# Performance work log

Hardware: AMD Instinct MI355X
Metric: run time of the kernel (lower is better)

Reference implementation:

```python
import jax, jax.numpy as jnp
import numpy as np

NEG_MAX = -jnp.finfo(jnp.float32).max


def apply_rotary(x):
    # x: (b, h, n, d) with d = key_dim; interleaved rotary (lucidrains rotary-embedding-torch)
    d = x.shape[-1]
    n = x.shape[-2]
    inv_freq = 1.0 / (10000.0 ** (jnp.arange(0, d, 2, dtype=jnp.float32) / d))
    t = jnp.arange(n, dtype=jnp.float32)
    freqs = t[:, None] * inv_freq[None, :]              # (n, d/2)
    cos, sin = jnp.cos(freqs), jnp.sin(freqs)
    x1, x2 = x[..., 0::2], x[..., 1::2]                 # even/odd interleaved pairs
    out1 = x1 * cos - x2 * sin
    out2 = x1 * sin + x2 * cos
    return jnp.stack([out1, out2], axis=-1).reshape(x.shape)


def setup_inputs() -> dict:
    key = jax.random.key(0)
    ks = jax.random.split(key, 12)
    b, n, dim, de = 2, 1024, 256, 64
    h, kd, vd = 8, 32, 32
    node_in = jax.random.normal(ks[0], (b, n, dim), dtype=jnp.float32)
    edge_in = jax.random.normal(ks[1], (b, n, n, de), dtype=jnp.float32)
    mask = jax.random.randint(ks[2], (b, n), 0, 2).astype(bool)
    s = 1.0 / np.sqrt(dim)
    Wq = jax.random.normal(ks[3], (dim, h * kd), dtype=jnp.float32) * s
    Wk = jax.random.normal(ks[4], (dim, h * kd), dtype=jnp.float32) * s
    Wv = jax.random.normal(ks[5], (dim, h * vd), dtype=jnp.float32) * s
    We = jax.random.normal(ks[6], (de, h), dtype=jnp.float32) * (1.0 / np.sqrt(de))
    be = jax.random.normal(ks[7], (h,), dtype=jnp.float32) * 0.01
    Wo = jax.random.normal(ks[8], (h * (vd + de), dim), dtype=jnp.float32) * (1.0 / np.sqrt(h * (vd + de)))
    bo = jax.random.normal(ks[9], (dim,), dtype=jnp.float32) * 0.01
    return {"node_in": node_in, "edge_in": edge_in, "mask": mask,
            "Wq": Wq, "Wk": Wk, "Wv": Wv, "We": We, "be": be, "Wo": Wo, "bo": bo}


def reference(node_in, edge_in, mask, Wq, Wk, Wv, We, be, Wo, bo):
    b, n, dim = node_in.shape
    h = be.shape[0]
    kd = Wq.shape[1] // h
    vd = Wv.shape[1] // h
    num_attn_logits = 2
    node_scale = (num_attn_logits * kd) ** -0.5
    edge_scale = num_attn_logits ** -0.5

    # projections -> (b, h, n, d)
    def proj(W, d):
        return (node_in @ W).reshape(b, n, h, d).transpose(0, 2, 1, 3)
    q, k, v = proj(Wq, kd), proj(Wk, kd), proj(Wv, vd)
    q, k = apply_rotary(q), apply_rotary(k)

    logits = jnp.einsum('bhid,bhjd->bhij', q, k) * node_scale
    edge_bias = (jnp.einsum('bijd,dh->bijh', edge_in, We) + be)  # (b, n, n, h)
    logits = logits + edge_bias.transpose(0, 3, 1, 2) * edge_scale

    pair_mask = mask[:, :, None] & mask[:, None, :]              # (b, n, n)
    logits = jnp.where(pair_mask[:, None, :, :], logits, NEG_MAX)

    attn = jax.nn.softmax(logits, axis=-1)                       # (b, h, n, n)

    res_node = jnp.einsum('bhij,bhjd->bhid', attn, v)            # (b, h, n, vd)
    res_edge = jnp.einsum('bhij,bijd->bhid', attn, edge_in)      # (b, h, n, de)

    res_node = res_node.transpose(0, 2, 1, 3).reshape(b, n, h * vd)
    res_edge = res_edge.transpose(0, 2, 1, 3).reshape(b, n, -1)
    out = jnp.concatenate([res_node, res_edge], axis=-1) @ Wo + bo
    return out
```

## Files before the change

kernel.cpp:

```cpp
#include <hip/hip_runtime.h>
#include <hip/hip_bf16.h>

typedef float f32x4 __attribute__((ext_vector_type(4)));
typedef short short8 __attribute__((ext_vector_type(8)));
typedef unsigned short u16;
typedef unsigned int u32;
typedef unsigned int u32x4 __attribute__((ext_vector_type(4)));

#define NEG_MAX (-3.4028234663852886e38f)
#define NODE_SCALE 0.125f
#define EDGE_SCALE 0.70710678118654752f
#define TSTR 68

__device__ __forceinline__ u16 f2bf(float f) {
  unsigned int x = __builtin_bit_cast(unsigned int, f);
  x = x + 0x7FFFu + ((x >> 16) & 1u);
  return (u16)(x >> 16);
}
__device__ __forceinline__ float asf(u32 x) { return __builtin_bit_cast(float, x); }
__device__ __forceinline__ u32 cvtpk(float lo, float hi) {
  u32 r;
  asm("v_cvt_pk_bf16_f32 %0, %1, %2" : "=v"(r) : "v"(lo), "v"(hi));
  return r;
}

__global__ void mask_norm(const unsigned char* __restrict__ mraw,
                          float* __restrict__ mask_f) {
  __shared__ int flags;
  int t = threadIdx.x;
  if (t == 0) flags = 0;
  __syncthreads();
  const unsigned int* mu = (const unsigned int*)mraw;
  int f = 0;
  for (int e = t; e < 512; e += 256) { if (mu[e] > 1u) f |= 1; }
  for (int e = t; e < 2048; e += 256) { if (mraw[e] > 1) f |= 2; }
  if (f) atomicOr(&flags, f);
  __syncthreads();
  int fl = flags;
  for (int e = t; e < 2048; e += 256) {
    float v;
    if (!(fl & 1))      v = (mu[e] != 0u) ? 1.f : 0.f;
    else if (!(fl & 2)) v = (mraw[e] != 0) ? 1.f : 0.f;
    else                v = (((const float*)mraw)[e] != 0.f) ? 1.f : 0.f;
    mask_f[e] = v;
  }
}

__global__ __launch_bounds__(256) void qkv_rope(
    const float* __restrict__ node, const float* __restrict__ Wq,
    const float* __restrict__ Wk, const float* __restrict__ Wv,
    float* __restrict__ qw, u16* __restrict__ kwb, u16* __restrict__ vwb) {
  __shared__ __align__(16) float xs[8 * 256];
  int t = threadIdx.x;
  int row0 = blockIdx.x * 8;
#pragma unroll
  for (int p = 0; p < 2; ++p) {
    int f = p * 256 + t;
    *(f32x4*)(&xs[f * 4]) = *(const f32x4*)(node + (size_t)row0 * 256 + f * 4);
  }
  __syncthreads();
  float qa[8], ka[8], va[8];
#pragma unroll
  for (int r = 0; r < 8; ++r) { qa[r] = 0.f; ka[r] = 0.f; va[r] = 0.f; }
  for (int c = 0; c < 256; ++c) {
    float wq = Wq[c * 256 + t];
    float wk = Wk[c * 256 + t];
    float wv = Wv[c * 256 + t];
#pragma unroll
    for (int r = 0; r < 8; ++r) {
      float x = xs[r * 256 + c];
      qa[r] += x * wq; ka[r] += x * wk; va[r] += x * wv;
    }
  }
  int d = t & 31;
  float inv = powf(10000.f, -((float)(2 * (d >> 1)) * (1.f / 32.f)));
  int h = t >> 5;
#pragma unroll
  for (int r = 0; r < 8; ++r) {
    int gr = row0 + r;
    int b = gr >> 10, i = gr & 1023;
    float ang = (float)i * inv;
    float sn, cs;
    sincosf(ang, &sn, &cs);
    float qp = __shfl_xor(qa[r], 1, 64);
    float kp = __shfl_xor(ka[r], 1, 64);
    float qo = (d & 1) ? (qp * sn + qa[r] * cs) : (qa[r] * cs - qp * sn);
    float ko = (d & 1) ? (kp * sn + ka[r] * cs) : (ka[r] * cs - kp * sn);
    int idx = ((b * 8 + h) * 1024 + i) * 32 + d;
    qw[idx] = qo;
    kwb[idx] = f2bf(ko);
    vwb[idx] = f2bf(va[r]);
  }
}

#define WREG 1280
__global__ __launch_bounds__(256) void attn_fused(
    const float* __restrict__ edge, const float* __restrict__ qw,
    const u16* __restrict__ kwb, const u16* __restrict__ vwb,
    const float* __restrict__ We, const float* __restrict__ be,
    const float* __restrict__ mask_f, float* __restrict__ rescat) {
  __shared__ __align__(16) float S[4 * WREG];

  int bid = blockIdx.x;
  int xcd = bid & 7, slot = bid >> 3;
  int b = xcd >> 2;
  int i = (xcd & 3) * 256 + slot;
  int t = threadIdx.x;
  int lane = t & 63;
  int w = __builtin_amdgcn_readfirstlane(t >> 6);

  float* tile = S + w * WREG;
  float* Pf = tile + 1088;
  float* Rg = tile + 1248;

  int j16 = lane & 15;
  int hq = lane >> 4;
  int hD = lane >> 3, sD = lane & 7;
  int jrl = lane >> 2, c4 = lane & 3;
  int jh = sD >> 2, do4 = sD & 3;

  float mi = mask_f[b * 1024 + i];
  u32 mb = 0;
  if (mi != 0.f) {
#pragma unroll
    for (int tt = 0; tt < 16; ++tt) {
      float v = mask_f[b * 1024 + tt * 64 + w * 16 + j16];
      mb |= (v != 0.f ? 1u : 0u) << tt;
    }
  }
  f32x4 besq = *(const f32x4*)(be + (hq & 1) * 4);
  besq *= EDGE_SCALE;

  short8 weA0, weA1;
  {
    int hh = lane & 15, g = lane >> 4;
#pragma unroll
    for (int e = 0; e < 8; ++e) {
      int d0 = g * 8 + e;
      float w0 = (hh < 8) ? We[d0 * 8 + hh] * EDGE_SCALE : 0.f;
      float w1 = (hh < 8) ? We[(d0 + 32) * 8 + hh] * EDGE_SCALE : 0.f;
      weA0[e] = (short)f2bf(w0);
      weA1[e] = (short)f2bf(w1);
    }
  }

  short8 qA[8];
  {
    int hh = (lane & 15) & 7;
    const float* qp = qw + ((size_t)((b * 8 + hh) * 1024 + i)) * 32 + (lane >> 4) * 8;
    f32x4 qv0 = *(const f32x4*)(qp);
    f32x4 qv1 = *(const f32x4*)(qp + 4);
    qv0 *= NODE_SCALE;
    qv1 *= NODE_SCALE;
    u32x4 qpk;
    qpk[0] = cvtpk(qv0.x, qv0.y); qpk[1] = cvtpk(qv0.z, qv0.w);
    qpk[2] = cvtpk(qv1.x, qv1.y); qpk[3] = cvtpk(qv1.z, qv1.w);
    u32x4 zz = {0u, 0u, 0u, 0u};
#pragma unroll
    for (int h = 0; h < 8; ++h)
      qA[h] = __builtin_bit_cast(short8, ((lane & 15) == h) ? qpk : zz);
  }

  const float* ebase = edge + ((size_t)(b * 1024 + i)) * (1024 * 64);
  const float* gsrc = ebase + (size_t)(w * 16 + jrl) * 64 + c4 * 16;
  float* wdst = tile + jrl * TSTR + c4 * 16;

  {
    f32x4 a0 = __builtin_nontemporal_load((const f32x4*)(gsrc + 0));
    f32x4 a1 = __builtin_nontemporal_load((const f32x4*)(gsrc + 4));
    f32x4 a2 = __builtin_nontemporal_load((const f32x4*)(gsrc + 8));
    f32x4 a3 = __builtin_nontemporal_load((const f32x4*)(gsrc + 12));
    *(f32x4*)(wdst + 0) = a0;
    *(f32x4*)(wdst + 4) = a1;
    *(f32x4*)(wdst + 8) = a2;
    *(f32x4*)(wdst + 12) = a3;
  }

  f32x4 vm = {NEG_MAX, NEG_MAX, NEG_MAX, NEG_MAX};
  f32x4 vs = {0.f, 0.f, 0.f, 0.f};
  f32x4 av0 = {0.f, 0.f, 0.f, 0.f}, av1 = {0.f, 0.f, 0.f, 0.f};
  f32x4 acce0 = {0.f, 0.f, 0.f, 0.f}, acce1 = {0.f, 0.f, 0.f, 0.f};
  f32x4 acce2 = {0.f, 0.f, 0.f, 0.f}, acce3 = {0.f, 0.f, 0.f, 0.f};

  for (int tt = 0; tt < 16; ++tt) {
    int j0 = tt * 64;
    bool pf = tt < 15;
    f32x4 st0, st1, st2, st3;
    if (pf) {
      const float* g = gsrc + (size_t)(j0 + 64) * 64;
      st0 = __builtin_nontemporal_load((const f32x4*)(g + 0));
      st1 = __builtin_nontemporal_load((const f32x4*)(g + 4));
      st2 = __builtin_nontemporal_load((const f32x4*)(g + 8));
      st3 = __builtin_nontemporal_load((const f32x4*)(g + 12));
    }

    f32x4 bacc = {0.f, 0.f, 0.f, 0.f};
    {
      const float* rp = tile + j16 * TSTR + hq * 8;
      f32x4 ea0 = *(const f32x4*)(rp + 0);
      f32x4 ea1 = *(const f32x4*)(rp + 4);
      f32x4 eb0 = *(const f32x4*)(rp + 32);
      f32x4 eb1 = *(const f32x4*)(rp + 36);
      u32x4 p0, p1;
      p0[0] = cvtpk(ea0.x, ea0.y); p0[1] = cvtpk(ea0.z, ea0.w);
      p0[2] = cvtpk(ea1.x, ea1.y); p0[3] = cvtpk(ea1.z, ea1.w);
      p1[0] = cvtpk(eb0.x, eb0.y); p1[1] = cvtpk(eb0.z, eb0.w);
      p1[2] = cvtpk(eb1.x, eb1.y); p1[3] = cvtpk(eb1.z, eb1.w);
      bacc = __builtin_amdgcn_mfma_f32_16x16x32_bf16(
          weA0, __builtin_bit_cast(short8, p0), bacc, 0, 0, 0);
      bacc = __builtin_amdgcn_mfma_f32_16x16x32_bf16(
          weA1, __builtin_bit_cast(short8, p1), bacc, 0, 0, 0);
    }
#pragma unroll
    for (int h = 0; h < 8; ++h) {
      const u16* kp = kwb + ((size_t)((b * 8 + h) * 1024 + j0 + w * 16 + j16)) * 32 + hq * 8;
      short8 kB = *(const short8*)kp;
      bacc = __builtin_amdgcn_mfma_f32_16x16x32_bf16(qA[h], kB, bacc, 0, 0, 0);
    }

    f32x4 p;
    {
      bool pm = (mb >> tt) & 1u;
      f32x4 l;
#pragma unroll
      for (int r = 0; r < 4; ++r) l[r] = pm ? (bacc[r] + besq[r]) : NEG_MAX;
      f32x4 mx = l;
#pragma unroll
      for (int off = 1; off < 16; off <<= 1) {
#pragma unroll
        for (int r = 0; r < 4; ++r) mx[r] = fmaxf(mx[r], __shfl_xor(mx[r], off, 64));
      }
      f32x4 mn, rs;
#pragma unroll
      for (int r = 0; r < 4; ++r) {
        mn[r] = fmaxf(vm[r], mx[r]);
        p[r] = __expf(l[r] - mn[r]);
      }
      f32x4 ps = p;
#pragma unroll
      for (int off = 1; off < 16; off <<= 1) {
#pragma unroll
        for (int r = 0; r < 4; ++r) ps[r] += __shfl_xor(ps[r], off, 64);
      }
#pragma unroll
      for (int r = 0; r < 4; ++r) rs[r] = __expf(vm[r] - mn[r]);
      vs = vs * rs + ps;
      vm = mn;
      if (lane < 32) {
        float* pw = Pf + hq * 80 + j16;
        pw[0] = p[0]; pw[20] = p[1]; pw[40] = p[2]; pw[60] = p[3];
        if (j16 == 0) *(f32x4*)(Rg + hq * 4) = rs;
      }
    }

    {
      float r = Rg[hD];
      const float* prow = Pf + hD * 20;
      f32x4 pr0 = *(const f32x4*)(prow + 0);
      f32x4 pr1 = *(const f32x4*)(prow + 4);
      f32x4 pr2 = *(const f32x4*)(prow + 8);
      f32x4 pr3 = *(const f32x4*)(prow + 12);
      const u16* vb = vwb + ((size_t)((b * 8 + hD) * 1024 + j0 + w * 16 + jh * 8)) * 32 + do4 * 8;
      f32x4 prA = jh ? pr2 : pr0, prB = jh ? pr3 : pr1;
      f32x4 sv0 = {0.f, 0.f, 0.f, 0.f}, sv1 = {0.f, 0.f, 0.f, 0.f};
#pragma unroll
      for (int x = 0; x < 8; ++x) {
        float pv = (x < 4) ? prA[x] : prB[x - 4];
        u32x4 vv = *(const u32x4*)(vb + (size_t)x * 32);
        f32x4 e0 = {asf(vv[0] << 16), asf(vv[0] & 0xffff0000u),
                    asf(vv[1] << 16), asf(vv[1] & 0xffff0000u)};
        f32x4 e1 = {asf(vv[2] << 16), asf(vv[2] & 0xffff0000u),
                    asf(vv[3] << 16), asf(vv[3] & 0xffff0000u)};
        sv0 += e0 * pv;
        sv1 += e1 * pv;
      }
      av0 = av0 * r + sv0;
      av1 = av1 * r + sv1;
    }

    {
      f32x4 rgv = *(const f32x4*)(Rg + (hq & 1) * 4);
      const float* pArow = Pf + (lane & 7) * 20 + (hq & 1) * 8;
      f32x4 pa0 = *(const f32x4*)(pArow);
      f32x4 pa1 = *(const f32x4*)(pArow + 4);
      u32x4 apk;
      apk[0] = cvtpk(pa0.x, pa0.y); apk[1] = cvtpk(pa0.z, pa0.w);
      apk[2] = cvtpk(pa1.x, pa1.y); apk[3] = cvtpk(pa1.z, pa1.w);
      if (hq >= 2) apk = (u32x4){0u, 0u, 0u, 0u};
      short8 pAf = __builtin_bit_cast(short8, apk);
      const float* cb = tile + (hq & 1) * 8 * TSTR + j16;
#define PE_STEP(ACC, NT) {                                                   \
      float b0 = cb[(NT)*16 + 0*TSTR], b1 = cb[(NT)*16 + 1*TSTR];            \
      float b2 = cb[(NT)*16 + 2*TSTR], b3 = cb[(NT)*16 + 3*TSTR];            \
      float b4 = cb[(NT)*16 + 4*TSTR], b5 = cb[(NT)*16 + 5*TSTR];            \
      float b6 = cb[(NT)*16 + 6*TSTR], b7 = cb[(NT)*16 + 7*TSTR];            \
      u32x4 bpk;                                                             \
      bpk[0] = cvtpk(b0, b1); bpk[1] = cvtpk(b2, b3);                        \
      bpk[2] = cvtpk(b4, b5); bpk[3] = cvtpk(b6, b7);                        \
      ACC = ACC * rgv;                                                       \
      ACC = __builtin_amdgcn_mfma_f32_16x16x32_bf16(                         \
          pAf, __builtin_bit_cast(short8, bpk), ACC, 0, 0, 0); }
      PE_STEP(acce0, 0)
      PE_STEP(acce1, 1)
      PE_STEP(acce2, 2)
      PE_STEP(acce3, 3)
#undef PE_STEP
    }

    if (pf) {
      *(f32x4*)(wdst + 0) = st0;
      *(f32x4*)(wdst + 4) = st1;
      *(f32x4*)(wdst + 8) = st2;
      *(f32x4*)(wdst + 12) = st3;
    }
  }

  __syncthreads();
  float* mrg = S + w * 1040;
  if (lane < 32) {
    int h0 = hq * 4;
    if (j16 == 0) {
#pragma unroll
      for (int r = 0; r < 4; ++r) { mrg[h0 + r] = vm[r]; mrg[8 + h0 + r] = vs[r]; }
    }
#pragma unroll
    for (int r = 0; r < 4; ++r) {
      mrg[528 + (h0 + r) * 64 + 0 + j16] = acce0[r];
      mrg[528 + (h0 + r) * 64 + 16 + j16] = acce1[r];
      mrg[528 + (h0 + r) * 64 + 32 + j16] = acce2[r];
      mrg[528 + (h0 + r) * 64 + 48 + j16] = acce3[r];
    }
  }
  *(f32x4*)(mrg + 16 + jh * 256 + hD * 32 + do4 * 8) = av0;
  *(f32x4*)(mrg + 16 + jh * 256 + hD * 32 + do4 * 8 + 4) = av1;
  __syncthreads();
  {
    int h = t >> 5, d = t & 31;
    float mx = fmaxf(fmaxf(S[h], S[1040 + h]), fmaxf(S[2080 + h], S[3120 + h]));
    float ew[4];
    float ssum = 0.f, vsum = 0.f;
#pragma unroll
    for (int ww = 0; ww < 4; ++ww) {
      const float* mw = S + ww * 1040;
      ew[ww] = __expf(mw[h] - mx);
      ssum += mw[8 + h] * ew[ww];
      vsum += (mw[16 + h * 32 + d] + mw[16 + 256 + h * 32 + d]) * ew[ww];
    }
    float inv = 1.f / ssum;
    size_t obase = ((size_t)(b * 1024 + i)) * 768;
    rescat[obase + h * 32 + d] = vsum * inv;
    float e0 = 0.f, e1 = 0.f;
#pragma unroll
    for (int ww = 0; ww < 4; ++ww) {
      const float* mw = S + ww * 1040;
      e0 += mw[528 + h * 64 + d] * ew[ww];
      e1 += mw[528 + h * 64 + 32 + d] * ew[ww];
    }
    rescat[obase + 256 + h * 64 + d] = e0 * inv;
    rescat[obase + 256 + h * 64 + 32 + d] = e1 * inv;
  }
}

__global__ __launch_bounds__(256) void out_proj(
    const float* __restrict__ rescat, const float* __restrict__ Wo,
    const float* __restrict__ bo, float* __restrict__ out) {
  __shared__ __align__(16) float xs[8 * 768];
  int t = threadIdx.x;
  int row0 = blockIdx.x * 8;
#pragma unroll
  for (int p = 0; p < 6; ++p) {
    int f = p * 256 + t;
    *(f32x4*)(&xs[f * 4]) = *(const f32x4*)(rescat + (size_t)row0 * 768 + f * 4);
  }
  __syncthreads();
  float acc[8];
#pragma unroll
  for (int r = 0; r < 8; ++r) acc[r] = 0.f;
  for (int c = 0; c < 768; ++c) {
    float w = Wo[c * 256 + t];
#pragma unroll
    for (int r = 0; r < 8; ++r) acc[r] += xs[r * 768 + c] * w;
  }
  float bias = bo[t];
#pragma unroll
  for (int r = 0; r < 8; ++r)
    out[(size_t)(row0 + r) * 256 + t] = acc[r] + bias;
}

extern "C" void kernel_launch(void* const* d_in, const int* in_sizes, int n_in,
                              void* d_out, int out_size, void* d_ws, size_t ws_size,
                              hipStream_t stream) {
  const float* node = (const float*)d_in[0];
  const float* edge = (const float*)d_in[1];
  const unsigned char* mask = (const unsigned char*)d_in[2];
  const float* Wq = (const float*)d_in[3];
  const float* Wk = (const float*)d_in[4];
  const float* Wv = (const float*)d_in[5];
  const float* We = (const float*)d_in[6];
  const float* be = (const float*)d_in[7];
  const float* Wo = (const float*)d_in[8];
  const float* bo = (const float*)d_in[9];

  float* ws = (float*)d_ws;
  float* qw = ws;
  u16* kwb = (u16*)(ws + 524288);
  u16* vwb = kwb + 524288;
  float* rescat = ws + 1048576;
  float* mask_f = ws + 2621440;

  hipLaunchKernelGGL(mask_norm, dim3(1), dim3(256), 0, stream, mask, mask_f);
  hipLaunchKernelGGL(qkv_rope, dim3(256), dim3(256), 0, stream,
                     node, Wq, Wk, Wv, qw, kwb, vwb);
  hipLaunchKernelGGL(attn_fused, dim3(2048), dim3(256), 0, stream,
                     edge, qw, kwb, vwb, We, be, mask_f, rescat);
  hipLaunchKernelGGL(out_proj, dim3(256), dim3(256), 0, stream,
                     rescat, Wo, bo, (float*)d_out);
}
```

Before: 393.8 us.

## Process two key tiles per online-softmax step with doubled edge prefetch

After: 402.3 us. 1.02x slower.

```diff
diff --git a/kernel.cpp b/kernel.cpp
--- a/kernel.cpp
+++ b/kernel.cpp
@@ -11,6 +11,8 @@
 #define NODE_SCALE 0.125f
 #define EDGE_SCALE 0.70710678118654752f
 #define TSTR 68
+#define PSTR 36
+#define WREG 2496
 
 __device__ __forceinline__ u16 f2bf(float f) {
   unsigned int x = __builtin_bit_cast(unsigned int, f);
@@ -93,7 +95,6 @@
   }
 }
 
-#define WREG 1280
 __global__ __launch_bounds__(256) void attn_fused(
     const float* __restrict__ edge, const float* __restrict__ qw,
     const u16* __restrict__ kwb, const u16* __restrict__ vwb,
@@ -109,9 +110,11 @@
   int lane = t & 63;
   int w = __builtin_amdgcn_readfirstlane(t >> 6);
 
-  float* tile = S + w * WREG;
-  float* Pf = tile + 1088;
-  float* Rg = tile + 1248;
+  float* base = S + w * WREG;
+  float* tA = base;
+  float* tB = base + 1088;
+  float* Pf = base + 2176;
+  float* Rg = base + 2464;
 
   int j16 = lane & 15;
   int hq = lane >> 4;
@@ -163,17 +166,23 @@
 
   const float* ebase = edge + ((size_t)(b * 1024 + i)) * (1024 * 64);
   const float* gsrc = ebase + (size_t)(w * 16 + jrl) * 64 + c4 * 16;
-  float* wdst = tile + jrl * TSTR + c4 * 16;
 
   {
     f32x4 a0 = __builtin_nontemporal_load((const f32x4*)(gsrc + 0));
     f32x4 a1 = __builtin_nontemporal_load((const f32x4*)(gsrc + 4));
     f32x4 a2 = __builtin_nontemporal_load((const f32x4*)(gsrc + 8));
     f32x4 a3 = __builtin_nontemporal_load((const f32x4*)(gsrc + 12));
-    *(f32x4*)(wdst + 0) = a0;
-    *(f32x4*)(wdst + 4) = a1;
-    *(f32x4*)(wdst + 8) = a2;
-    *(f32x4*)(wdst + 12) = a3;
+    const float* g2 = gsrc + 64 * 64;
+    f32x4 b0 = __builtin_nontemporal_load((const f32x4*)(g2 + 0));
+    f32x4 b1 = __builtin_nontemporal_load((const f32x4*)(g2 + 4));
+    f32x4 b2 = __builtin_nontemporal_load((const f32x4*)(g2 + 8));
+    f32x4 b3 = __builtin_nontemporal_load((const f32x4*)(g2 + 12));
+    float* wa = tA + jrl * TSTR + c4 * 16;
+    float* wb = tB + jrl * TSTR + c4 * 16;
+    *(f32x4*)(wa + 0) = a0; *(f32x4*)(wa + 4) = a1;
+    *(f32x4*)(wa + 8) = a2; *(f32x4*)(wa + 12) = a3;
+    *(f32x4*)(wb + 0) = b0; *(f32x4*)(wb + 4) = b1;
+    *(f32x4*)(wb + 8) = b2; *(f32x4*)(wb + 12) = b3;
   }
 
   f32x4 vm = {NEG_MAX, NEG_MAX, NEG_MAX, NEG_MAX};
@@ -182,21 +191,31 @@
   f32x4 acce0 = {0.f, 0.f, 0.f, 0.f}, acce1 = {0.f, 0.f, 0.f, 0.f};
   f32x4 acce2 = {0.f, 0.f, 0.f, 0.f}, acce3 = {0.f, 0.f, 0.f, 0.f};
 
-  for (int tt = 0; tt < 16; ++tt) {
-    int j0 = tt * 64;
-    bool pf = tt < 15;
-    f32x4 st0, st1, st2, st3;
+  for (int m = 0; m < 8; ++m) {
+    int j0 = m * 128;
+    bool pf = m < 7;
+    f32x4 sA0, sA1, sA2, sA3, sB0, sB1, sB2, sB3;
     if (pf) {
-      const float* g = gsrc + (size_t)(j0 + 64) * 64;
-      st0 = __builtin_nontemporal_load((const f32x4*)(g + 0));
-      st1 = __builtin_nontemporal_load((const f32x4*)(g + 4));
-      st2 = __builtin_nontemporal_load((const f32x4*)(g + 8));
-      st3 = __builtin_nontemporal_load((const f32x4*)(g + 12));
-    }
-
-    f32x4 bacc = {0.f, 0.f, 0.f, 0.f};
+      const float* gA = gsrc + (size_t)(j0 + 128) * 64;
+      const float* gB = gsrc + (size_t)(j0 + 192) * 64;
+      sA0 = __builtin_nontemporal_load((const f32x4*)(gA + 0));
+      sA1 = __builtin_nontemporal_load((const f32x4*)(gA + 4));
+      sA2 = __builtin_nontemporal_load((const f32x4*)(gA + 8));
+      sA3 = __builtin_nontemporal_load((const f32x4*)(gA + 12));
+      sB0 = __builtin_nontemporal_load((const f32x4*)(gB + 0));
+      sB1 = __builtin_nontemporal_load((const f32x4*)(gB + 4));
+      sB2 = __builtin_nontemporal_load((const f32x4*)(gB + 8));
+      sB3 = __builtin_nontemporal_load((const f32x4*)(gB + 12));
+    }
+
+    short8 kA[8];
+#pragma unroll
+    for (int h = 0; h < 8; ++h)
+      kA[h] = *(const short8*)(kwb +
+          ((size_t)((b * 8 + h) * 1024 + j0 + w * 16 + j16)) * 32 + hq * 8);
+    f32x4 baccA = {0.f, 0.f, 0.f, 0.f};
     {
-      const float* rp = tile + j16 * TSTR + hq * 8;
+      const float* rp = tA + j16 * TSTR + hq * 8;
       f32x4 ea0 = *(const f32x4*)(rp + 0);
       f32x4 ea1 = *(const f32x4*)(rp + 4);
       f32x4 eb0 = *(const f32x4*)(rp + 32);
@@ -206,37 +225,64 @@
       p0[2] = cvtpk(ea1.x, ea1.y); p0[3] = cvtpk(ea1.z, ea1.w);
       p1[0] = cvtpk(eb0.x, eb0.y); p1[1] = cvtpk(eb0.z, eb0.w);
       p1[2] = cvtpk(eb1.x, eb1.y); p1[3] = cvtpk(eb1.z, eb1.w);
-      bacc = __builtin_amdgcn_mfma_f32_16x16x32_bf16(
-          weA0, __builtin_bit_cast(short8, p0), bacc, 0, 0, 0);
-      bacc = __builtin_amdgcn_mfma_f32_16x16x32_bf16(
-          weA1, __builtin_bit_cast(short8, p1), bacc, 0, 0, 0);
-    }
-#pragma unroll
-    for (int h = 0; h < 8; ++h) {
-      const u16* kp = kwb + ((size_t)((b * 8 + h) * 1024 + j0 + w * 16 + j16)) * 32 + hq * 8;
-      short8 kB = *(const short8*)kp;
-      bacc = __builtin_amdgcn_mfma_f32_16x16x32_bf16(qA[h], kB, bacc, 0, 0, 0);
-    }
-
-    f32x4 p;
+      baccA = __builtin_amdgcn_mfma_f32_16x16x32_bf16(
+          weA0, __builtin_bit_cast(short8, p0), baccA, 0, 0, 0);
+      baccA = __builtin_amdgcn_mfma_f32_16x16x32_bf16(
+          weA1, __builtin_bit_cast(short8, p1), baccA, 0, 0, 0);
+    }
+#pragma unroll
+    for (int h = 0; h < 8; ++h)
+      baccA = __builtin_amdgcn_mfma_f32_16x16x32_bf16(qA[h], kA[h], baccA, 0, 0, 0);
+
+    short8 kB[8];
+#pragma unroll
+    for (int h = 0; h < 8; ++h)
+      kB[h] = *(const short8*)(kwb +
+          ((size_t)((b * 8 + h) * 1024 + j0 + 64 + w * 16 + j16)) * 32 + hq * 8);
+    f32x4 baccB = {0.f, 0.f, 0.f, 0.f};
     {
-      bool pm = (mb >> tt) & 1u;
-      f32x4 l;
-#pragma unroll
-      for (int r = 0; r < 4; ++r) l[r] = pm ? (bacc[r] + besq[r]) : NEG_MAX;
-      f32x4 mx = l;
+      const float* rp = tB + j16 * TSTR + hq * 8;
+      f32x4 ea0 = *(const f32x4*)(rp + 0);
+      f32x4 ea1 = *(const f32x4*)(rp + 4);
+      f32x4 eb0 = *(const f32x4*)(rp + 32);
+      f32x4 eb1 = *(const f32x4*)(rp + 36);
+      u32x4 p0, p1;
+      p0[0] = cvtpk(ea0.x, ea0.y); p0[1] = cvtpk(ea0.z, ea0.w);
+      p0[2] = cvtpk(ea1.x, ea1.y); p0[3] = cvtpk(ea1.z, ea1.w);
+      p1[0] = cvtpk(eb0.x, eb0.y); p1[1] = cvtpk(eb0.z, eb0.w);
+      p1[2] = cvtpk(eb1.x, eb1.y); p1[3] = cvtpk(eb1.z, eb1.w);
+      baccB = __builtin_amdgcn_mfma_f32_16x16x32_bf16(
+          weA0, __builtin_bit_cast(short8, p0), baccB, 0, 0, 0);
+      baccB = __builtin_amdgcn_mfma_f32_16x16x32_bf16(
+          weA1, __builtin_bit_cast(short8, p1), baccB, 0, 0, 0);
+    }
+#pragma unroll
+    for (int h = 0; h < 8; ++h)
+      baccB = __builtin_amdgcn_mfma_f32_16x16x32_bf16(qA[h], kB[h], baccB, 0, 0, 0);
+
+    {
+      bool pmA = (mb >> (2 * m)) & 1u;
+      bool pmB = (mb >> (2 * m + 1)) & 1u;
+      f32x4 lA, lB, pA, pB, mx;
+#pragma unroll
+      for (int r = 0; r < 4; ++r) {
+        lA[r] = pmA ? (baccA[r] + besq[r]) : NEG_MAX;
+        lB[r] = pmB ? (baccB[r] + besq[r]) : NEG_MAX;
+        mx[r] = fmaxf(lA[r], lB[r]);
+      }
 #pragma unroll
       for (int off = 1; off < 16; off <<= 1) {
 #pragma unroll
         for (int r = 0; r < 4; ++r) mx[r] = fmaxf(mx[r], __shfl_xor(mx[r], off, 64));
       }
-      f32x4 mn, rs;
+      f32x4 mn, rs, ps;
 #pragma unroll
       for (int r = 0; r < 4; ++r) {
         mn[r] = fmaxf(vm[r], mx[r]);
-        p[r] = __expf(l[r] - mn[r]);
-      }
-      f32x4 ps = p;
+        pA[r] = __expf(lA[r] - mn[r]);
+        pB[r] = __expf(lB[r] - mn[r]);
+        ps[r] = pA[r] + pB[r];
+      }
 #pragma unroll
       for (int off = 1; off < 16; off <<= 1) {
 #pragma unroll
@@ -247,26 +293,35 @@
       vs = vs * rs + ps;
       vm = mn;
       if (lane < 32) {
-        float* pw = Pf + hq * 80 + j16;
-        pw[0] = p[0]; pw[20] = p[1]; pw[40] = p[2]; pw[60] = p[3];
+        float* pw = Pf + hq * (4 * PSTR) + j16;
+        pw[0 * PSTR] = pA[0]; pw[1 * PSTR] = pA[1];
+        pw[2 * PSTR] = pA[2]; pw[3 * PSTR] = pA[3];
+        pw[0 * PSTR + 16] = pB[0]; pw[1 * PSTR + 16] = pB[1];
+        pw[2 * PSTR + 16] = pB[2]; pw[3 * PSTR + 16] = pB[3];
         if (j16 == 0) *(f32x4*)(Rg + hq * 4) = rs;
       }
     }
 
     {
       float r = Rg[hD];
-      const float* prow = Pf + hD * 20;
-      f32x4 pr0 = *(const f32x4*)(prow + 0);
-      f32x4 pr1 = *(const f32x4*)(prow + 4);
-      f32x4 pr2 = *(const f32x4*)(prow + 8);
-      f32x4 pr3 = *(const f32x4*)(prow + 12);
-      const u16* vb = vwb + ((size_t)((b * 8 + hD) * 1024 + j0 + w * 16 + jh * 8)) * 32 + do4 * 8;
-      f32x4 prA = jh ? pr2 : pr0, prB = jh ? pr3 : pr1;
+      const float* prow = Pf + hD * PSTR;
+      f32x4 a0 = *(const f32x4*)(prow + 0);
+      f32x4 a1 = *(const f32x4*)(prow + 4);
+      f32x4 a2 = *(const f32x4*)(prow + 8);
+      f32x4 a3 = *(const f32x4*)(prow + 12);
+      f32x4 b0 = *(const f32x4*)(prow + 16);
+      f32x4 b1 = *(const f32x4*)(prow + 20);
+      f32x4 b2 = *(const f32x4*)(prow + 24);
+      f32x4 b3 = *(const f32x4*)(prow + 28);
+      f32x4 prA = jh ? a2 : a0, prA2 = jh ? a3 : a1;
+      f32x4 prB = jh ? b2 : b0, prB2 = jh ? b3 : b1;
+      const u16* vbA = vwb + ((size_t)((b * 8 + hD) * 1024 + j0 + w * 16 + jh * 8)) * 32 + do4 * 8;
+      const u16* vbB = vbA + (size_t)64 * 32;
       f32x4 sv0 = {0.f, 0.f, 0.f, 0.f}, sv1 = {0.f, 0.f, 0.f, 0.f};
 #pragma unroll
       for (int x = 0; x < 8; ++x) {
-        float pv = (x < 4) ? prA[x] : prB[x - 4];
-        u32x4 vv = *(const u32x4*)(vb + (size_t)x * 32);
+        float pv = (x < 4) ? prA[x] : prA2[x - 4];
+        u32x4 vv = *(const u32x4*)(vbA + (size_t)x * 32);
         f32x4 e0 = {asf(vv[0] << 16), asf(vv[0] & 0xffff0000u),
                     asf(vv[1] << 16), asf(vv[1] & 0xffff0000u)};
         f32x4 e1 = {asf(vv[2] << 16), asf(vv[2] & 0xffff0000u),
@@ -274,44 +329,72 @@
         sv0 += e0 * pv;
         sv1 += e1 * pv;
       }
+#pragma unroll
+      for (int x = 0; x < 8; ++x) {
+        float pv = (x < 4) ? prB[x] : prB2[x - 4];
+        u32x4 vv = *(const u32x4*)(vbB + (size_t)x * 32);
+        f32x4 e0 = {asf(vv[0] << 16), asf(vv[0] & 0xffff0000u),
+                    asf(vv[1] << 16), asf(vv[1] & 0xffff0000u)};
+        f32x4 e1 = {asf(vv[2] << 16), asf(vv[2] & 0xffff0000u),
+                    asf(vv[3] << 16), asf(vv[3] & 0xffff0000u)};
+        sv0 += e0 * pv;
+        sv1 += e1 * pv;
+      }
       av0 = av0 * r + sv0;
       av1 = av1 * r + sv1;
     }
 
     {
       f32x4 rgv = *(const f32x4*)(Rg + (hq & 1) * 4);
-      const float* pArow = Pf + (lane & 7) * 20 + (hq & 1) * 8;
-      f32x4 pa0 = *(const f32x4*)(pArow);
-      f32x4 pa1 = *(const f32x4*)(pArow + 4);
-      u32x4 apk;
-      apk[0] = cvtpk(pa0.x, pa0.y); apk[1] = cvtpk(pa0.z, pa0.w);
-      apk[2] = cvtpk(pa1.x, pa1.y); apk[3] = cvtpk(pa1.z, pa1.w);
-      if (hq >= 2) apk = (u32x4){0u, 0u, 0u, 0u};
-      short8 pAf = __builtin_bit_cast(short8, apk);
-      const float* cb = tile + (hq & 1) * 8 * TSTR + j16;
-#define PE_STEP(ACC, NT) {                                                   \
-      float b0 = cb[(NT)*16 + 0*TSTR], b1 = cb[(NT)*16 + 1*TSTR];            \
-      float b2 = cb[(NT)*16 + 2*TSTR], b3 = cb[(NT)*16 + 3*TSTR];            \
-      float b4 = cb[(NT)*16 + 4*TSTR], b5 = cb[(NT)*16 + 5*TSTR];            \
-      float b6 = cb[(NT)*16 + 6*TSTR], b7 = cb[(NT)*16 + 7*TSTR];            \
-      u32x4 bpk;                                                             \
-      bpk[0] = cvtpk(b0, b1); bpk[1] = cvtpk(b2, b3);                        \
-      bpk[2] = cvtpk(b4, b5); bpk[3] = cvtpk(b6, b7);                        \
+      const float* pAr = Pf + (lane & 7) * PSTR + (hq & 1) * 8;
+      f32x4 pa0 = *(const f32x4*)(pAr);
+      f32x4 pa1 = *(const f32x4*)(pAr + 4);
+      f32x4 pb0 = *(const f32x4*)(pAr + 16);
+      f32x4 pb1 = *(const f32x4*)(pAr + 20);
+      u32x4 apkA, apkB;
+      apkA[0] = cvtpk(pa0.x, pa0.y); apkA[1] = cvtpk(pa0.z, pa0.w);
+      apkA[2] = cvtpk(pa1.x, pa1.y); apkA[3] = cvtpk(pa1.z, pa1.w);
+      apkB[0] = cvtpk(pb0.x, pb0.y); apkB[1] = cvtpk(pb0.z, pb0.w);
+      apkB[2] = cvtpk(pb1.x, pb1.y); apkB[3] = cvtpk(pb1.z, pb1.w);
+      if (hq >= 2) { apkA = (u32x4){0u,0u,0u,0u}; apkB = (u32x4){0u,0u,0u,0u}; }
+      short8 pAfA = __builtin_bit_cast(short8, apkA);
+      short8 pAfB = __builtin_bit_cast(short8, apkB);
+      const float* cbA = tA + (hq & 1) * 8 * TSTR + j16;
+      const float* cbB = tB + (hq & 1) * 8 * TSTR + j16;
+#define PE_STEP2(ACC, NT) {                                                  \
+      float a0_ = cbA[(NT)*16 + 0*TSTR], a1_ = cbA[(NT)*16 + 1*TSTR];        \
+      float a2_ = cbA[(NT)*16 + 2*TSTR], a3_ = cbA[(NT)*16 + 3*TSTR];        \
+      float a4_ = cbA[(NT)*16 + 4*TSTR], a5_ = cbA[(NT)*16 + 5*TSTR];        \
+      float a6_ = cbA[(NT)*16 + 6*TSTR], a7_ = cbA[(NT)*16 + 7*TSTR];        \
+      u32x4 bka;                                                             \
+      bka[0] = cvtpk(a0_, a1_); bka[1] = cvtpk(a2_, a3_);                    \
+      bka[2] = cvtpk(a4_, a5_); bka[3] = cvtpk(a6_, a7_);                    \
+      float b0_ = cbB[(NT)*16 + 0*TSTR], b1_ = cbB[(NT)*16 + 1*TSTR];        \
+      float b2_ = cbB[(NT)*16 + 2*TSTR], b3_ = cbB[(NT)*16 + 3*TSTR];        \
+      float b4_ = cbB[(NT)*16 + 4*TSTR], b5_ = cbB[(NT)*16 + 5*TSTR];        \
+      float b6_ = cbB[(NT)*16 + 6*TSTR], b7_ = cbB[(NT)*16 + 7*TSTR];        \
+      u32x4 bkb;                                                             \
+      bkb[0] = cvtpk(b0_, b1_); bkb[1] = cvtpk(b2_, b3_);                    \
+      bkb[2] = cvtpk(b4_, b5_); bkb[3] = cvtpk(b6_, b7_);                    \
       ACC = ACC * rgv;                                                       \
       ACC = __builtin_amdgcn_mfma_f32_16x16x32_bf16(                         \
-          pAf, __builtin_bit_cast(short8, bpk), ACC, 0, 0, 0); }
-      PE_STEP(acce0, 0)
-      PE_STEP(acce1, 1)
-      PE_STEP(acce2, 2)
-      PE_STEP(acce3, 3)
-#undef PE_STEP
+          pAfA, __builtin_bit_cast(short8, bka), ACC, 0, 0, 0);              \
+      ACC = __builtin_amdgcn_mfma_f32_16x16x32_bf16(                         \
+          pAfB, __builtin_bit_cast(short8, bkb), ACC, 0, 0, 0); }
+      PE_STEP2(acce0, 0)
+      PE_STEP2(acce1, 1)
+      PE_STEP2(acce2, 2)
+      PE_STEP2(acce3, 3)
+#undef PE_STEP2
     }
 
     if (pf) {
-      *(f32x4*)(wdst + 0) = st0;
-      *(f32x4*)(wdst + 4) = st1;
-      *(f32x4*)(wdst + 8) = st2;
-      *(f32x4*)(wdst + 12) = st3;
+      float* wa = tA + jrl * TSTR + c4 * 16;
+      float* wb = tB + jrl * TSTR + c4 * 16;
+      *(f32x4*)(wa + 0) = sA0; *(f32x4*)(wa + 4) = sA1;
+      *(f32x4*)(wa + 8) = sA2; *(f32x4*)(wa + 12) = sA3;
+      *(f32x4*)(wb + 0) = sB0; *(f32x4*)(wb + 4) = sB1;
+      *(f32x4*)(wb + 8) = sB2; *(f32x4*)(wb + 12) = sB3;
     }
   }
 
```
